# Kernel tuning notes

Hardware: AMD Instinct MI355X
Metric: run time of the kernel (lower is better)

Reference implementation:

```python
import jax, jax.numpy as jnp
import numpy as np

D_K = 64
MASK_FILL = -1e9


def setup_inputs() -> dict:
    key = jax.random.key(0)
    kq, kk, kv, km = jax.random.split(key, 4)
    B, H, S, D = 2, 16, 2048, D_K
    q = jax.random.normal(kq, (B, H, S, D), dtype=jnp.float32)
    k = jax.random.normal(kk, (B, H, D, S), dtype=jnp.float32)  # pre-transposed keys
    v = jax.random.normal(kv, (B, H, S, D), dtype=jnp.float32)
    mask = jax.random.randint(km, (B, H, S, S), 0, 2).astype(jnp.bool_)
    return {"q": q, "k": k, "v": v, "mask": mask}


def reference(q, k, v, mask):
    # scores: [B, H, S, S] = q @ k (k already [B,H,D,S])
    scores = jnp.einsum("bhsd,bhdt->bhst", q, k) / jnp.sqrt(jnp.float32(D_K))
    scores = jnp.where(mask, MASK_FILL, scores)
    attn = jax.nn.softmax(scores, axis=-1)
    context = jnp.einsum("bhst,bhtd->bhsd", attn, v)
    return (context, attn)
```

## Files before the change

### kernel.cpp

```cpp
#include <hip/hip_runtime.h>

#define S_LEN    2048
#define DK       64
#define N_BH     32
#define ROWS     16
#define NTHREADS 512

typedef float          f32x4  __attribute__((ext_vector_type(4)));
typedef int            i32x4  __attribute__((ext_vector_type(4)));
typedef short          bf16x8 __attribute__((ext_vector_type(8)));
typedef unsigned short u16x8  __attribute__((ext_vector_type(8)));
typedef unsigned int   u32x4  __attribute__((ext_vector_type(4)));

__device__ __forceinline__ unsigned short f2bf(float f) {
    unsigned u = __builtin_bit_cast(unsigned, f);
    u += 0x7fffu + ((u >> 16) & 1u);
    return (unsigned short)(u >> 16);
}
__device__ __forceinline__ float bf2f(unsigned short h) {
    unsigned u = ((unsigned)h) << 16;
    return __builtin_bit_cast(float, u);
}
__device__ __forceinline__ unsigned pack_bf2(float a, float b) {
    return (unsigned)f2bf(a) | ((unsigned)f2bf(b) << 16);
}

__global__ void prep_qcast(const float* __restrict__ q, unsigned short* __restrict__ Qb) {
    const long i = ((long)blockIdx.x * 256 + threadIdx.x) * 8;
    f32x4 a = *(const f32x4*)(q + i);
    f32x4 b = *(const f32x4*)(q + i + 4);
    u16x8 o;
    o[0]=f2bf(a.x); o[1]=f2bf(a.y); o[2]=f2bf(a.z); o[3]=f2bf(a.w);
    o[4]=f2bf(b.x); o[5]=f2bf(b.y); o[6]=f2bf(b.z); o[7]=f2bf(b.w);
    *(u16x8*)(Qb + i) = o;
}

__global__ void prep_k(const float* __restrict__ k, unsigned short* __restrict__ Kb) {
    __shared__ float t[64][65];
    const int bh = blockIdx.x >> 5, s0 = (blockIdx.x & 31) << 6;
    const int tx = threadIdx.x;
    const float* kb = k + (long)bh * 64 * S_LEN;
    #pragma unroll
    for (int i = 0; i < 16; ++i) {
        const int d = (i << 2) + (tx >> 6), s = tx & 63;
        t[d][s] = kb[(long)d * S_LEN + s0 + s];
    }
    __syncthreads();
    #pragma unroll
    for (int i = 0; i < 16; ++i) {
        const int s = (i << 2) + (tx >> 6), d = tx & 63;
        Kb[((long)bh * S_LEN + s0 + s) * DK + d] = f2bf(t[d][s]);
    }
}

__global__ void prep_v(const float* __restrict__ v, unsigned short* __restrict__ Vb) {
    __shared__ float t[64][65];
    const int bh = blockIdx.x >> 5, s0 = (blockIdx.x & 31) << 6;
    const int tx = threadIdx.x;
    #pragma unroll
    for (int i = 0; i < 16; ++i) {
        const int s = (i << 2) + (tx >> 6), d = tx & 63;
        t[s][d] = v[((long)bh * S_LEN + s0 + s) * DK + d];
    }
    __syncthreads();
    #pragma unroll
    for (int i = 0; i < 16; ++i) {
        const int d = (i << 2) + (tx >> 6), s = tx & 63;
        Vb[((long)bh * DK + d) * S_LEN + s0 + s] = f2bf(t[s][d]);
    }
}

template <bool WS>
__global__ __launch_bounds__(NTHREADS, 4)
void sdpa_main(const float* __restrict__ q, const float* __restrict__ k,
               const float* __restrict__ v, const int* __restrict__ mask,
               const unsigned short* __restrict__ Qb,
               const unsigned short* __restrict__ Kb,
               const unsigned short* __restrict__ Vb,
               float* __restrict__ ctx, float* __restrict__ attn)
{
    __shared__ float rowsum[ROWS];
    __shared__ float ctxlds[ROWS * DK];

    const int bid  = blockIdx.x;
    const int bh   = bid & (N_BH - 1);
    const int qt   = bid >> 5;
    const int tid  = threadIdx.x;
    const int wave = tid >> 6;
    const int lane = tid & 63;
    const int m    = lane & 15;
    const int g    = lane >> 4;
    const long rowbase = (long)bh * S_LEN + qt * ROWS;

    if (tid < ROWS) rowsum[tid] = 0.0f;
    for (int i = tid; i < ROWS * DK; i += NTHREADS) ctxlds[i] = 0.0f;
    __syncthreads();

    unsigned P0[16], P1[16];
    float rsum = 0.0f;

    {
        bf16x8 qfrag[2];
        if (WS) {
            const unsigned short* qp = Qb + (rowbase + m) * DK;
            qfrag[0] = *(const bf16x8*)(qp + g * 8);
            qfrag[1] = *(const bf16x8*)(qp + 32 + g * 8);
        } else {
            const float* qp = q + (rowbase + m) * DK;
            #pragma unroll
            for (int ks = 0; ks < 2; ++ks) {
                const float* p = qp + ks * 32 + g * 8;
                f32x4 x0 = *(const f32x4*)p, x1 = *(const f32x4*)(p + 4);
                qfrag[ks][0]=(short)f2bf(x0.x); qfrag[ks][1]=(short)f2bf(x0.y);
                qfrag[ks][2]=(short)f2bf(x0.z); qfrag[ks][3]=(short)f2bf(x0.w);
                qfrag[ks][4]=(short)f2bf(x1.x); qfrag[ks][5]=(short)f2bf(x1.y);
                qfrag[ks][6]=(short)f2bf(x1.z); qfrag[ks][7]=(short)f2bf(x1.w);
            }
        }
        const int tw = wave << 8;
        const long mrow = (rowbase + m) * (long)S_LEN;
        #pragma unroll
        for (int ct = 0; ct < 16; ++ct) {
            const int t0 = tw + (ct << 4);
            const int tk = t0 + m;
            const i32x4 mk = *(const i32x4*)(mask + mrow + t0 + (g << 2));
            f32x4 acc = {0.f, 0.f, 0.f, 0.f};
            #pragma unroll
            for (int ks = 0; ks < 2; ++ks) {
                bf16x8 kfrag;
                if (WS) {
                    kfrag = *(const bf16x8*)(Kb + ((long)bh * S_LEN + tk) * DK + ks * 32 + g * 8);
                } else {
                    const float* kp = k + (long)bh * DK * S_LEN + (long)(ks * 32 + g * 8) * S_LEN + tk;
                    #pragma unroll
                    for (int j = 0; j < 8; ++j) kfrag[j] = (short)f2bf(kp[(long)j * S_LEN]);
                }
                acc = __builtin_amdgcn_mfma_f32_16x16x32_bf16(kfrag, qfrag[ks], acc, 0, 0, 0);
            }
            const float e0 = mk.x ? 0.0f : __expf(acc[0] * 0.125f);
            const float e1 = mk.y ? 0.0f : __expf(acc[1] * 0.125f);
            const float e2 = mk.z ? 0.0f : __expf(acc[2] * 0.125f);
            const float e3 = mk.w ? 0.0f : __expf(acc[3] * 0.125f);
            rsum += (e0 + e1) + (e2 + e3);
            P0[ct] = pack_bf2(e0, e1);
            P1[ct] = pack_bf2(e2, e3);
        }
        rsum += __shfl_xor(rsum, 16);
        rsum += __shfl_xor(rsum, 32);
        if (lane < 16) atomicAdd(&rowsum[lane], rsum);
    }
    __syncthreads();
    const float rinv = 1.0f / rowsum[m];

    {
        f32x4 cacc[4] = { {0,0,0,0}, {0,0,0,0}, {0,0,0,0}, {0,0,0,0} };
        const int tw   = wave << 8;
        const int srcA = ((g & 1) << 5) + m;
        const int srcB = srcA + 16;
        const int hi   = g >> 1;
        float* aout = attn + (rowbase + m) * (long)S_LEN;
        #pragma unroll
        for (int kt = 0; kt < 8; ++kt) {
            #pragma unroll
            for (int h = 0; h < 2; ++h) {
                const int ct = 2 * kt + h;
                const unsigned lo = P0[ct], hp = P1[ct];
                f32x4 o = { bf2f((unsigned short)(lo & 0xFFFF)) * rinv,
                            bf2f((unsigned short)(lo >> 16))    * rinv,
                            bf2f((unsigned short)(hp & 0xFFFF)) * rinv,
                            bf2f((unsigned short)(hp >> 16))    * rinv };
                __builtin_nontemporal_store(o, (f32x4*)(aout + tw + (ct << 4) + (g << 2)));
            }
            const unsigned a0e = (unsigned)__shfl((int)P0[2*kt],   srcA);
            const unsigned a0o = (unsigned)__shfl((int)P0[2*kt+1], srcA);
            const unsigned a1e = (unsigned)__shfl((int)P1[2*kt],   srcA);
            const unsigned a1o = (unsigned)__shfl((int)P1[2*kt+1], srcA);
            const unsigned a2e = (unsigned)__shfl((int)P0[2*kt],   srcB);
            const unsigned a2o = (unsigned)__shfl((int)P0[2*kt+1], srcB);
            const unsigned a3e = (unsigned)__shfl((int)P1[2*kt],   srcB);
            const unsigned a3o = (unsigned)__shfl((int)P1[2*kt+1], srcB);
            u32x4 wv = { hi ? a0o : a0e, hi ? a1o : a1e,
                         hi ? a2o : a2e, hi ? a3o : a3e };
            const bf16x8 af = __builtin_bit_cast(bf16x8, wv);
            const int tb = tw + (kt << 5) + (g << 3);
            #pragma unroll
            for (int dt = 0; dt < 4; ++dt) {
                bf16x8 bfv;
                if (WS) {
                    bfv = *(const bf16x8*)(Vb + ((long)bh * DK + dt * 16 + m) * S_LEN + tb);
                } else {
                    const float* vp = v + ((long)bh * S_LEN + tb) * DK + dt * 16 + m;
                    #pragma unroll
                    for (int j = 0; j < 8; ++j) bfv[j] = (short)f2bf(vp[j * DK]);
                }
                cacc[dt] = __builtin_amdgcn_mfma_f32_16x16x32_bf16(af, bfv, cacc[dt], 0, 0, 0);
            }
        }
        #pragma unroll
        for (int dt = 0; dt < 4; ++dt)
            #pragma unroll
            for (int i = 0; i < 4; ++i)
                atomicAdd(&ctxlds[(4 * g + i) * DK + dt * 16 + m], cacc[dt][i]);
    }
    __syncthreads();

    #pragma unroll
    for (int i = tid; i < ROWS * DK; i += NTHREADS) {
        const int rr = i >> 6, dd = i & 63;
        ctx[(rowbase + rr) * DK + dd] = ctxlds[i] / rowsum[rr];
    }
}

extern "C" void kernel_launch(void* const* d_in, const int* in_sizes, int n_in,
                              void* d_out, int out_size, void* d_ws, size_t ws_size,
                              hipStream_t stream)
{
    const float* q    = (const float*)d_in[0];
    const float* k    = (const float*)d_in[1];
    const float* v    = (const float*)d_in[2];
    const int*   mask = (const int*)d_in[3];

    float* ctx  = (float*)d_out;
    float* attn = ctx + (size_t)N_BH * S_LEN * DK;

    const size_t nel = (size_t)N_BH * S_LEN * DK;
    const bool use_ws = ws_size >= nel * 3 * sizeof(unsigned short);
    unsigned short* Qb = (unsigned short*)d_ws;
    unsigned short* Kb = Qb + nel;
    unsigned short* Vb = Kb + nel;

    const int nblocks = N_BH * (S_LEN / ROWS);

    if (use_ws) {
        prep_qcast<<<(int)(nel / (256 * 8)), 256, 0, stream>>>(q, Qb);
        prep_k<<<N_BH * (S_LEN / 64), 256, 0, stream>>>(k, Kb);
        prep_v<<<N_BH * (S_LEN / 64), 256, 0, stream>>>(v, Vb);
        sdpa_main<true><<<nblocks, NTHREADS, 0, stream>>>(q, k, v, mask, Qb, Kb, Vb, ctx, attn);
    } else {
        sdpa_main<false><<<nblocks, NTHREADS, 0, stream>>>(q, k, v, mask,
                                                           nullptr, nullptr, nullptr, ctx, attn);
    }
}
```

Before: 489.1 us.

## Fuse softmax numerator with PV MFMA, apply mask in A-fragment layout

Merges the QK/exp phase and the P·V MFMA phase into a single loop, so unnormalized probabilities feed the context accumulation straight away and the barrier between the two phases is gone. The mask is now read as 8 contiguous ints per lane in the PV A-fragment layout and applied to the packed bf16 values, and the row sum is taken from those masked values. Attention output stores move after the only barrier and write 32-byte contiguous runs per lane. The risks are higher register pressure from holding AF plus four accumulators, and a row sum now built from bf16-rounded values.

```diff
diff --git a/kernel.cpp b/kernel.cpp
--- a/kernel.cpp
+++ b/kernel.cpp
@@ -96,34 +96,41 @@
     for (int i = tid; i < ROWS * DK; i += NTHREADS) ctxlds[i] = 0.0f;
     __syncthreads();
 
-    unsigned P0[16], P1[16];
+    bf16x8 qfrag[2];
+    if (WS) {
+        const unsigned short* qp = Qb + (rowbase + m) * DK;
+        qfrag[0] = *(const bf16x8*)(qp + g * 8);
+        qfrag[1] = *(const bf16x8*)(qp + 32 + g * 8);
+    } else {
+        const float* qp = q + (rowbase + m) * DK;
+        #pragma unroll
+        for (int ks = 0; ks < 2; ++ks) {
+            const float* p = qp + ks * 32 + g * 8;
+            f32x4 x0 = *(const f32x4*)p, x1 = *(const f32x4*)(p + 4);
+            qfrag[ks][0]=(short)f2bf(x0.x); qfrag[ks][1]=(short)f2bf(x0.y);
+            qfrag[ks][2]=(short)f2bf(x0.z); qfrag[ks][3]=(short)f2bf(x0.w);
+            qfrag[ks][4]=(short)f2bf(x1.x); qfrag[ks][5]=(short)f2bf(x1.y);
+            qfrag[ks][6]=(short)f2bf(x1.z); qfrag[ks][7]=(short)f2bf(x1.w);
+        }
+    }
+
+    const int tw   = wave << 8;
+    const int srcA = ((g & 1) << 5) + m;
+    const int srcB = srcA + 16;
+    const int hi   = g >> 1;
+    const int* mrow = mask + (rowbase + m) * (long)S_LEN;
+
+    u32x4 AF[8];
+    f32x4 cacc0 = {0,0,0,0}, cacc1 = {0,0,0,0}, cacc2 = {0,0,0,0}, cacc3 = {0,0,0,0};
     float rsum = 0.0f;
 
-    {
-        bf16x8 qfrag[2];
-        if (WS) {
-            const unsigned short* qp = Qb + (rowbase + m) * DK;
-            qfrag[0] = *(const bf16x8*)(qp + g * 8);
-            qfrag[1] = *(const bf16x8*)(qp + 32 + g * 8);
-        } else {
-            const float* qp = q + (rowbase + m) * DK;
-            #pragma unroll
-            for (int ks = 0; ks < 2; ++ks) {
-                const float* p = qp + ks * 32 + g * 8;
-                f32x4 x0 = *(const f32x4*)p, x1 = *(const f32x4*)(p + 4);
-                qfrag[ks][0]=(short)f2bf(x0.x); qfrag[ks][1]=(short)f2bf(x0.y);
-                qfrag[ks][2]=(short)f2bf(x0.z); qfrag[ks][3]=(short)f2bf(x0.w);
-                qfrag[ks][4]=(short)f2bf(x1.x); qfrag[ks][5]=(short)f2bf(x1.y);
-                qfrag[ks][6]=(short)f2bf(x1.z); qfrag[ks][7]=(short)f2bf(x1.w);
-            }
-        }
-        const int tw = wave << 8;
-        const long mrow = (rowbase + m) * (long)S_LEN;
-        #pragma unroll
-        for (int ct = 0; ct < 16; ++ct) {
-            const int t0 = tw + (ct << 4);
+    #pragma unroll
+    for (int kt = 0; kt < 8; ++kt) {
+        unsigned pk0e, pk1e, pk0o, pk1o;
+        #pragma unroll
+        for (int h = 0; h < 2; ++h) {
+            const int t0 = tw + ((2 * kt + h) << 4);
             const int tk = t0 + m;
-            const i32x4 mk = *(const i32x4*)(mask + mrow + t0 + (g << 2));
             f32x4 acc = {0.f, 0.f, 0.f, 0.f};
             #pragma unroll
             for (int ks = 0; ks < 2; ++ks) {
@@ -137,72 +144,84 @@
                 }
                 acc = __builtin_amdgcn_mfma_f32_16x16x32_bf16(kfrag, qfrag[ks], acc, 0, 0, 0);
             }
-            const float e0 = mk.x ? 0.0f : __expf(acc[0] * 0.125f);
-            const float e1 = mk.y ? 0.0f : __expf(acc[1] * 0.125f);
-            const float e2 = mk.z ? 0.0f : __expf(acc[2] * 0.125f);
-            const float e3 = mk.w ? 0.0f : __expf(acc[3] * 0.125f);
-            rsum += (e0 + e1) + (e2 + e3);
-            P0[ct] = pack_bf2(e0, e1);
-            P1[ct] = pack_bf2(e2, e3);
-        }
-        rsum += __shfl_xor(rsum, 16);
-        rsum += __shfl_xor(rsum, 32);
-        if (lane < 16) atomicAdd(&rowsum[lane], rsum);
-    }
-    __syncthreads();
-    const float rinv = 1.0f / rowsum[m];
+            const float e0 = __expf(acc[0] * 0.125f);
+            const float e1 = __expf(acc[1] * 0.125f);
+            const float e2 = __expf(acc[2] * 0.125f);
+            const float e3 = __expf(acc[3] * 0.125f);
+            if (h == 0) { pk0e = pack_bf2(e0, e1); pk1e = pack_bf2(e2, e3); }
+            else        { pk0o = pack_bf2(e0, e1); pk1o = pack_bf2(e2, e3); }
+        }
+        const unsigned a0e = (unsigned)__shfl((int)pk0e, srcA);
+        const unsigned a0o = (unsigned)__shfl((int)pk0o, srcA);
+        const unsigned a1e = (unsigned)__shfl((int)pk1e, srcA);
+        const unsigned a1o = (unsigned)__shfl((int)pk1o, srcA);
+        const unsigned a2e = (unsigned)__shfl((int)pk0e, srcB);
+        const unsigned a2o = (unsigned)__shfl((int)pk0o, srcB);
+        const unsigned a3e = (unsigned)__shfl((int)pk1e, srcB);
+        const unsigned a3o = (unsigned)__shfl((int)pk1o, srcB);
+        u32x4 wv = { hi ? a0o : a0e, hi ? a1o : a1e,
+                     hi ? a2o : a2e, hi ? a3o : a3e };
+        const int tb = tw + (kt << 5) + (g << 3);
+        const i32x4 mk0 = *(const i32x4*)(mrow + tb);
+        const i32x4 mk1 = *(const i32x4*)(mrow + tb + 4);
+        if (mk0.x) wv.x &= 0xFFFF0000u;  if (mk0.y) wv.x &= 0x0000FFFFu;
+        if (mk0.z) wv.y &= 0xFFFF0000u;  if (mk0.w) wv.y &= 0x0000FFFFu;
+        if (mk1.x) wv.z &= 0xFFFF0000u;  if (mk1.y) wv.z &= 0x0000FFFFu;
+        if (mk1.z) wv.w &= 0xFFFF0000u;  if (mk1.w) wv.w &= 0x0000FFFFu;
+        AF[kt] = wv;
+        rsum += ((bf2f((unsigned short)(wv.x & 0xFFFF)) + bf2f((unsigned short)(wv.x >> 16)))
+               + (bf2f((unsigned short)(wv.y & 0xFFFF)) + bf2f((unsigned short)(wv.y >> 16))))
+              + ((bf2f((unsigned short)(wv.z & 0xFFFF)) + bf2f((unsigned short)(wv.z >> 16)))
+               + (bf2f((unsigned short)(wv.w & 0xFFFF)) + bf2f((unsigned short)(wv.w >> 16))));
+        const bf16x8 af = __builtin_bit_cast(bf16x8, wv);
+        #pragma unroll
+        for (int dt = 0; dt < 4; ++dt) {
+            bf16x8 bfv;
+            if (WS) {
+                bfv = *(const bf16x8*)(Vb + ((long)bh * DK + dt * 16 + m) * S_LEN + tb);
+            } else {
+                const float* vp = v + ((long)bh * S_LEN + tb) * DK + dt * 16 + m;
+                #pragma unroll
+                for (int j = 0; j < 8; ++j) bfv[j] = (short)f2bf(vp[j * DK]);
+            }
+            if      (dt == 0) cacc0 = __builtin_amdgcn_mfma_f32_16x16x32_bf16(af, bfv, cacc0, 0, 0, 0);
+            else if (dt == 1) cacc1 = __builtin_amdgcn_mfma_f32_16x16x32_bf16(af, bfv, cacc1, 0, 0, 0);
+            else if (dt == 2) cacc2 = __builtin_amdgcn_mfma_f32_16x16x32_bf16(af, bfv, cacc2, 0, 0, 0);
+            else              cacc3 = __builtin_amdgcn_mfma_f32_16x16x32_bf16(af, bfv, cacc3, 0, 0, 0);
+        }
+    }
+
+    rsum += __shfl_xor(rsum, 16);
+    rsum += __shfl_xor(rsum, 32);
+    if (lane < 16) atomicAdd(&rowsum[lane], rsum);
+    #pragma unroll
+    for (int i = 0; i < 4; ++i) {
+        atomicAdd(&ctxlds[(4 * g + i) * DK +  0 + m], cacc0[i]);
+        atomicAdd(&ctxlds[(4 * g + i) * DK + 16 + m], cacc1[i]);
+        atomicAdd(&ctxlds[(4 * g + i) * DK + 32 + m], cacc2[i]);
+        atomicAdd(&ctxlds[(4 * g + i) * DK + 48 + m], cacc3[i]);
+    }
+    __syncthreads();
 
     {
-        f32x4 cacc[4] = { {0,0,0,0}, {0,0,0,0}, {0,0,0,0}, {0,0,0,0} };
-        const int tw   = wave << 8;
-        const int srcA = ((g & 1) << 5) + m;
-        const int srcB = srcA + 16;
-        const int hi   = g >> 1;
+        const float rinv = 1.0f / rowsum[m];
         float* aout = attn + (rowbase + m) * (long)S_LEN;
         #pragma unroll
         for (int kt = 0; kt < 8; ++kt) {
-            #pragma unroll
-            for (int h = 0; h < 2; ++h) {
-                const int ct = 2 * kt + h;
-                const unsigned lo = P0[ct], hp = P1[ct];
-                f32x4 o = { bf2f((unsigned short)(lo & 0xFFFF)) * rinv,
-                            bf2f((unsigned short)(lo >> 16))    * rinv,
-                            bf2f((unsigned short)(hp & 0xFFFF)) * rinv,
-                            bf2f((unsigned short)(hp >> 16))    * rinv };
-                __builtin_nontemporal_store(o, (f32x4*)(aout + tw + (ct << 4) + (g << 2)));
-            }
-            const unsigned a0e = (unsigned)__shfl((int)P0[2*kt],   srcA);
-            const unsigned a0o = (unsigned)__shfl((int)P0[2*kt+1], srcA);
-            const unsigned a1e = (unsigned)__shfl((int)P1[2*kt],   srcA);
-            const unsigned a1o = (unsigned)__shfl((int)P1[2*kt+1], srcA);
-            const unsigned a2e = (unsigned)__shfl((int)P0[2*kt],   srcB);
-            const unsigned a2o = (unsigned)__shfl((int)P0[2*kt+1], srcB);
-            const unsigned a3e = (unsigned)__shfl((int)P1[2*kt],   srcB);
-            const unsigned a3o = (unsigned)__shfl((int)P1[2*kt+1], srcB);
-            u32x4 wv = { hi ? a0o : a0e, hi ? a1o : a1e,
-                         hi ? a2o : a2e, hi ? a3o : a3e };
-            const bf16x8 af = __builtin_bit_cast(bf16x8, wv);
+            const u32x4 wv = AF[kt];
             const int tb = tw + (kt << 5) + (g << 3);
-            #pragma unroll
-            for (int dt = 0; dt < 4; ++dt) {
-                bf16x8 bfv;
-                if (WS) {
-                    bfv = *(const bf16x8*)(Vb + ((long)bh * DK + dt * 16 + m) * S_LEN + tb);
-                } else {
-                    const float* vp = v + ((long)bh * S_LEN + tb) * DK + dt * 16 + m;
-                    #pragma unroll
-                    for (int j = 0; j < 8; ++j) bfv[j] = (short)f2bf(vp[j * DK]);
-                }
-                cacc[dt] = __builtin_amdgcn_mfma_f32_16x16x32_bf16(af, bfv, cacc[dt], 0, 0, 0);
-            }
-        }
-        #pragma unroll
-        for (int dt = 0; dt < 4; ++dt)
-            #pragma unroll
-            for (int i = 0; i < 4; ++i)
-                atomicAdd(&ctxlds[(4 * g + i) * DK + dt * 16 + m], cacc[dt][i]);
-    }
-    __syncthreads();
+            f32x4 o0 = { bf2f((unsigned short)(wv.x & 0xFFFF)) * rinv,
+                         bf2f((unsigned short)(wv.x >> 16))    * rinv,
+                         bf2f((unsigned short)(wv.y & 0xFFFF)) * rinv,
+                         bf2f((unsigned short)(wv.y >> 16))    * rinv };
+            f32x4 o1 = { bf2f((unsigned short)(wv.z & 0xFFFF)) * rinv,
+                         bf2f((unsigned short)(wv.z >> 16))    * rinv,
+                         bf2f((unsigned short)(wv.w & 0xFFFF)) * rinv,
+                         bf2f((unsigned short)(wv.w >> 16))    * rinv };
+            __builtin_nontemporal_store(o0, (f32x4*)(aout + tb));
+            __builtin_nontemporal_store(o1, (f32x4*)(aout + tb + 4));
+        }
+    }
 
     #pragma unroll
     for (int i = tid; i < ROWS * DK; i += NTHREADS) {
```

New measurement: 499.3 us. 2.1% more time.
